# Performance work log

Hardware: AMD Instinct MI355X
Metric: run time of the kernel (lower is better)

Reference implementation:

```python
import jax, jax.numpy as jnp
import numpy as np

TEMP = 1.0
MEM = 1000           # memory_size
DIM = 128            # embedding_dim
MARGIN = 0.2
NC = 21              # num_classes
HARD_RATIO = 0.8
K_EASY = int(MEM // 5 * (1 - HARD_RATIO))   # 40
K_HARD = int(MEM // 5 * HARD_RATIO)         # 160
A = K_EASY + K_HARD                          # 200 sampled anchors
EPS = 1e-8


def _nearest_down(x, h, w):
    # torch F.interpolate(mode='nearest') downscale: src = floor(dst*H_in/H_out)
    B, H, W = x.shape
    ri = jnp.arange(h) * H // h
    ci = jnp.arange(w) * W // w
    return x[:, ri[:, None], ci[None, :]]


def _pick_first(mask, k):
    # deterministic stand-in for sampling_mask: first k True indices
    n = mask.shape[0]
    score = jnp.where(mask, -jnp.arange(n, dtype=jnp.float32), -jnp.inf)
    _, idx = jax.lax.top_k(score, k)
    return idx, mask[idx]


def setup_inputs() -> dict:
    key = jax.random.key(0)
    ks = jax.random.split(key, 5)
    return {
        "preds": jax.random.normal(ks[0], (8, NC, 512, 512), jnp.float32),
        "embeddings": jax.random.normal(ks[1], (8, DIM, 128, 128), jnp.float32),
        "wsss_gts": jax.random.randint(ks[2], (8, 512, 512), 0, NC, jnp.int32),
        "fsss_gts": jax.random.randint(ks[3], (8, 512, 512), 0, NC, jnp.int32),
        "memory": jax.random.normal(ks[4], (NC - 1, MEM, DIM), jnp.float32),
    }


def reference(preds, embeddings, wsss_gts, fsss_gts, memory):
    B, D, h, w = embeddings.shape
    s_wsss = _nearest_down(wsss_gts, h, w).reshape(-1)                    # [N]
    s_pred = _nearest_down(preds.argmax(axis=1), h, w).reshape(-1)        # [N]
    s_fsss = _nearest_down(fsss_gts, h, w).reshape(-1)                    # [N]

    # L2-normalize embeddings over channel dim, flatten to [N, D]
    emb = embeddings / jnp.maximum(
        jnp.linalg.norm(embeddings, axis=1, keepdims=True), 1e-12)
    emb = emb.transpose(1, 0, 2, 3).reshape(D, -1).T                       # [N, D]

    fg = (s_fsss != 0) & (s_fsss != 255)
    valid_lbl = (s_wsss != 0) & (s_wsss != 255)
    # original loop body overwrites cls with the FIRST (smallest) fg class
    cls = jnp.min(jnp.where(valid_lbl, s_wsss, NC)).astype(jnp.int32)

    anc = (s_wsss == cls) & fg
    easy = anc & (s_pred == cls)
    hard = anc & ~(s_pred == cls)
    ei, ev = _pick_first(easy, K_EASY)
    hi, hv = _pick_first(hard, K_HARD)
    idx = jnp.concatenate([ei, hi])                                        # [A]
    valid = jnp.concatenate([ev, hv])                                      # [A]
    anchors = emb[idx]                                                     # [A, D] (unit norm)

    mem_n = memory / jnp.maximum(
        jnp.linalg.norm(memory, axis=-1, keepdims=True), EPS)
    # all anchor-vs-memory cosine similarities in one batched matmul
    sims = jnp.einsum('ad,cmd->acm', anchors, mem_n)                       # [A, NC-1, MEM]
    pos = sims[:, cls - 1, :]                                              # [A, MEM]
    neg_mask = (jnp.arange(NC - 1) != (cls - 1))
    neg = jnp.where(neg_mask[None, :, None], sims, -jnp.inf).reshape(A, -1)
    hard_neg, _ = jax.lax.top_k(neg, MEM)                                  # [A, MEM] hardest

    # all (pos, hard_neg) pairs per anchor: relu(pos - neg + margin)
    pair = jnp.maximum(pos[:, :, None] - hard_neg[:, None, :] + MARGIN, 0.0)  # [A,MEM,MEM]
    per_anchor = pair.mean(axis=(1, 2))
    vf = valid.astype(pair.dtype)
    loss = jnp.sum(per_anchor * vf) / jnp.maximum(jnp.sum(vf), 1.0)

    # circular memory update for class `cls` (ptr starts at 0); invalid -> dropped
    wpos = jnp.cumsum(valid.astype(jnp.int32)) - 1
    widx = jnp.where(valid, wpos % MEM, MEM)
    new_memory = memory.at[cls - 1, widx].set(
        jax.lax.stop_gradient(anchors), mode='drop')
    return loss, new_memory
```

## Files before the change

### kernel.cpp

```cpp
#include <hip/hip_runtime.h>
#include <stdint.h>

#define NCK 21
#define K_EASY 39
#define K_HARD 160
#define A_TOT  199
#define MARGINF 0.2f

#define OFF_EASY   64
#define OFF_HARD   256
#define OFF_PERA   1024
#define OFF_MINARR 2048
#define OFF_FLAGS1 4096
#define OFF_FLAGS2 135168
#define OFF_ANCH   266240
#define OFF_SIMS   409600

__device__ __forceinline__ unsigned int f2key(float f) {
  unsigned int u = __float_as_uint(f);
  return u ^ ((u & 0x80000000u) ? 0xFFFFFFFFu : 0x80000000u);
}
__device__ __forceinline__ float key2f(unsigned int k) {
  unsigned int u = (k & 0x80000000u) ? (k ^ 0x80000000u) : (k ^ 0xFFFFFFFFu);
  return __uint_as_float(u);
}

__global__ void k_prep(const int* __restrict__ wsss, const int* __restrict__ fsss,
                       unsigned char* __restrict__ flags1, int* __restrict__ minArr) {
  int p = blockIdx.x * 256 + threadIdx.x;
  int b = p >> 14, r = p & 16383, i = r >> 7, j = r & 127;
  int gi = (b * 512 + i * 4) * 512 + j * 4;
  int w = wsss[gi];
  int f = fsss[gi];
  int fg = (f != 0 && f != 255) ? 1 : 0;
  int wl = (w != 0 && w != 255) ? 1 : 0;
  flags1[p] = (unsigned char)((w & 63) | (fg << 6));
  int cand = wl ? w : NCK;
  for (int off = 32; off > 0; off >>= 1) cand = min(cand, __shfl_down(cand, off));
  __shared__ int wmin[4];
  int lane = threadIdx.x & 63, wid = threadIdx.x >> 6;
  if (lane == 0) wmin[wid] = cand;
  __syncthreads();
  if (threadIdx.x == 0)
    minArr[blockIdx.x] = min(min(wmin[0], wmin[1]), min(wmin[2], wmin[3]));
}

__global__ void k_flags(const float* __restrict__ preds, const unsigned char* __restrict__ flags1,
                        unsigned char* __restrict__ flags2, const int* __restrict__ minArr,
                        int* __restrict__ hdr) {
  int tid = threadIdx.x;
  __shared__ int wm[4];
  __shared__ int s_cls;
  int m = min(minArr[tid], minArr[tid + 256]);
  for (int off = 32; off > 0; off >>= 1) m = min(m, __shfl_down(m, off));
  int lane = tid & 63, wid = tid >> 6;
  if (lane == 0) wm[wid] = m;
  __syncthreads();
  if (tid == 0) {
    int c = min(min(wm[0], wm[1]), min(wm[2], wm[3]));
    s_cls = c;
    if (blockIdx.x == 0) { hdr[0] = c; hdr[6] = 0; }
  }
  __syncthreads();
  int cls = s_cls;
  int p = blockIdx.x * 256 + tid;
  unsigned char f1 = flags1[p];
  unsigned char out = 0;
  if ((f1 & 64) && (int)(f1 & 63) == cls) {
    int b = p >> 14, r = p & 16383, i = r >> 7, j = r & 127;
    int base = ((b * NCK) * 512 + i * 4) * 512 + j * 4;
    float best = preds[base]; int bi = 0;
#pragma unroll
    for (int ch = 1; ch < NCK; ++ch) {
      float v = preds[base + ch * 262144];
      if (v > best) { best = v; bi = ch; }
    }
    out = (bi == cls) ? 1 : 2;
  }
  flags2[p] = out;
}

__global__ void k_pick(const unsigned char* __restrict__ flags2, int* __restrict__ hdr,
                       int* __restrict__ easy_idx, int* __restrict__ hard_idx) {
  int lane = threadIdx.x;
  const unsigned long long* f8 = (const unsigned long long*)flags2;
  unsigned int runE = 0, runH = 0;
  for (int it4 = 0; it4 < 64; ++it4) {
    unsigned long long vv0 = f8[(it4 * 4 + 0) * 64 + lane];
    unsigned long long vv1 = f8[(it4 * 4 + 1) * 64 + lane];
    unsigned long long vv2 = f8[(it4 * 4 + 2) * 64 + lane];
    unsigned long long vv3 = f8[(it4 * 4 + 3) * 64 + lane];
#pragma unroll
    for (int q = 0; q < 4; ++q) {
      unsigned long long v = (q == 0) ? vv0 : (q == 1) ? vv1 : (q == 2) ? vv2 : vv3;
      int it = it4 * 4 + q;
      unsigned int e = 0, h = 0;
#pragma unroll
      for (int g = 0; g < 8; ++g) {
        unsigned int b = (unsigned int)((v >> (8 * g)) & 255ull);
        e += (b == 1u); h += (b == 2u);
      }
      unsigned int x = (e << 16) | h;
      unsigned int incl = x;
#pragma unroll
      for (int off = 1; off < 64; off <<= 1) {
        unsigned int t = __shfl_up(incl, off);
        if (lane >= off) incl += t;
      }
      unsigned int excl = incl - x;
      unsigned int eRk = runE + (excl >> 16);
      unsigned int hRk = runH + (excl & 0xFFFFu);
#pragma unroll
      for (int g = 0; g < 8; ++g) {
        unsigned int b = (unsigned int)((v >> (8 * g)) & 255ull);
        int p = it * 512 + lane * 8 + g;
        if (b == 1u)      { if (eRk < K_EASY) easy_idx[eRk] = p; eRk++; }
        else if (b == 2u) { if (hRk < K_HARD) hard_idx[hRk] = p; hRk++; }
      }
      unsigned int tot = __shfl(incl, 63);
      runE += (tot >> 16); runH += (tot & 0xFFFFu);
    }
    if (runE >= K_EASY && runH >= K_HARD) break;
  }
  if (lane == 0) {
    int neU = runE < K_EASY ? (int)runE : K_EASY;
    int nhU = runH < K_HARD ? (int)runH : K_HARD;
    hdr[1] = (int)runE; hdr[2] = (int)runH;
    hdr[3] = neU; hdr[4] = nhU; hdr[5] = neU + nhU;
  }
}

__global__ void k_anchors(const float* __restrict__ emb, const int* __restrict__ hdr,
                          const int* __restrict__ easy_idx, const int* __restrict__ hard_idx,
                          float* __restrict__ anchors) {
  int a = blockIdx.x;
  int tid = threadIdx.x;
  int nv = hdr[5], neU = hdr[3];
  float v0 = 0.f, v1 = 0.f;
  if (a < nv) {
    int p = (a < neU) ? easy_idx[a] : hard_idx[a - neU];
    int b = p >> 14, r = p & 16383, i = r >> 7, j = r & 127;
    int base = b * 2097152 + i * 128 + j;
    v0 = emb[base + tid * 16384];
    v1 = emb[base + (tid + 64) * 16384];
  }
  float ss = v0 * v0 + v1 * v1;
  for (int off = 32; off > 0; off >>= 1) ss += __shfl_xor(ss, off);
  float inv = 1.0f / fmaxf(sqrtf(ss), 1e-12f);
  anchors[a * 128 + tid] = v0 * inv;
  anchors[a * 128 + tid + 64] = v1 * inv;
}

__global__ __launch_bounds__(256) void k_sims(const float* __restrict__ anchors,
                       const float* __restrict__ memory, float* __restrict__ sims,
                       int a0, int ac) {
  __shared__ float As[64 * 128];
  __shared__ float Ms[64 * 128];
  int mT = blockIdx.x, aT = blockIdx.y;
  int aBase = aT * 64, mBase = mT * 64;
  int tid = threadIdx.x;
#pragma unroll
  for (int k = 0; k < 8; ++k) {
    int f4i = tid + k * 256;
    int row = f4i >> 5, c = f4i & 31;
    int gR = a0 + aBase + row; if (gR > 255) gR = 255;
    float4 v = ((const float4*)anchors)[gR * 32 + c];
    *(float4*)&As[row * 128 + ((c ^ (row & 31)) << 2)] = v;
  }
#pragma unroll
  for (int k = 0; k < 8; ++k) {
    int f4i = tid + k * 256;
    int row = f4i >> 5, c = f4i & 31;
    int grow = mBase + row;
    float4 v = make_float4(0.f, 0.f, 0.f, 0.f);
    if (grow < 20000) v = ((const float4*)memory)[grow * 32 + c];
    *(float4*)&Ms[row * 128 + ((c ^ (row & 31)) << 2)] = v;
  }
  __syncthreads();
  int tx = tid & 15, ty = tid >> 4;
  float acc[4][4];
#pragma unroll
  for (int i = 0; i < 4; ++i)
#pragma unroll
    for (int j = 0; j < 4; ++j) acc[i][j] = 0.f;
#pragma unroll 2
  for (int c = 0; c < 32; ++c) {
    float4 av[4], mv[4];
#pragma unroll
    for (int i = 0; i < 4; ++i) {
      int ar = ty + 16 * i;
      av[i] = *(const float4*)&As[ar * 128 + ((c ^ (ar & 31)) << 2)];
    }
#pragma unroll
    for (int j = 0; j < 4; ++j) {
      int mr = tx + 16 * j;
      mv[j] = *(const float4*)&Ms[mr * 128 + ((c ^ (mr & 31)) << 2)];
    }
#pragma unroll
    for (int i = 0; i < 4; ++i)
#pragma unroll
      for (int j = 0; j < 4; ++j)
        acc[i][j] += av[i].x * mv[j].x + av[i].y * mv[j].y + av[i].z * mv[j].z + av[i].w * mv[j].w;
  }
  __syncthreads();
  {
    int row = tid >> 2, q = tid & 3;
    float ss = 0.f;
#pragma unroll
    for (int k = 0; k < 8; ++k) {
      float4 v = *(const float4*)&Ms[row * 128 + q * 32 + k * 4];
      ss += v.x * v.x + v.y * v.y + v.z * v.z + v.w * v.w;
    }
    ss += __shfl_down(ss, 2, 4);
    ss += __shfl_down(ss, 1, 4);
    if (q == 0) As[row] = 1.0f / fmaxf(sqrtf(ss), 1e-8f);
  }
  __syncthreads();
#pragma unroll
  for (int i = 0; i < 4; ++i) {
    int la = aBase + ty + 16 * i;
    if (la < ac) {
#pragma unroll
      for (int j = 0; j < 4; ++j) {
        int m = mBase + tx + 16 * j;
        if (m < 20000) sims[(size_t)la * 20000 + m] = acc[i][j] * As[tx + 16 * j];
      }
    }
  }
}

__device__ __forceinline__ void suffix_select(unsigned int* histL, unsigned int* sfx,
                                              unsigned int* cnts, int tid, unsigned int krem) {
  if (tid < 64) {
    int lane = tid;
    unsigned int h0 = histL[lane * 4 + 0];
    unsigned int h1 = histL[lane * 4 + 1];
    unsigned int h2 = histL[lane * 4 + 2];
    unsigned int h3 = histL[lane * 4 + 3];
    unsigned int s = h0 + h1 + h2 + h3;
    unsigned int incl = s;
#pragma unroll
    for (int off = 1; off < 64; off <<= 1) {
      unsigned int t = __shfl_down(incl, off);
      if (lane + off < 64) incl += t;
    }
    unsigned int above = incl - s;
    unsigned int f3 = above + h3;
    unsigned int f2 = f3 + h2;
    unsigned int f1 = f2 + h1;
    unsigned int f0 = f1 + h0;
    sfx[lane * 4 + 0] = f0; sfx[lane * 4 + 1] = f1;
    sfx[lane * 4 + 2] = f2; sfx[lane * 4 + 3] = f3;
    if (lane == 63) sfx[256] = 0u;
    if (f0 >= krem && f1 < krem)    cnts[3] = (unsigned int)(lane * 4 + 0);
    if (f1 >= krem && f2 < krem)    cnts[3] = (unsigned int)(lane * 4 + 1);
    if (f2 >= krem && f3 < krem)    cnts[3] = (unsigned int)(lane * 4 + 2);
    if (f3 >= krem && above < krem) cnts[3] = (unsigned int)(lane * 4 + 3);
  }
  __syncthreads();
}

__global__ __launch_bounds__(1024) void k_topk(const float* __restrict__ sims,
                       int* __restrict__ hdr, float* __restrict__ per_anchor,
                       int a0, int ac, float* __restrict__ out,
                       const float* __restrict__ memory, const float* __restrict__ anchors,
                       int doCopy) {
  int tid = threadIdx.x, lane = tid & 63, wid = tid >> 6;
  int nv = hdr[5];
  int cls = hdr[0];

  if (doCopy) {
    int step = gridDim.x * 1024;
    for (int i = blockIdx.x * 1024 + tid; i < 2560000; i += step) {
      float v = memory[i];
      int c = i / 128000;
      int rem = i - c * 128000;
      int m = rem >> 7, d = rem & 127;
      if (cls >= 1 && cls <= 20 && c == cls - 1 && m < nv) v = anchors[m * 128 + d];
      out[1 + i] = v;
    }
    if (nv == 0 && blockIdx.x == 0 && tid == 0) out[0] = 0.f;
  }

  int la = blockIdx.x;
  if (la >= ac) return;
  int a = a0 + la;
  if (a >= nv) return;
  int clsRow = cls - 1;

  __shared__ float posArr[1024];
  __shared__ float qv[1024];
  __shared__ unsigned int hist16[16][256];
  __shared__ unsigned int histL[256];
  __shared__ unsigned int sfx[257];
  __shared__ unsigned int buf[12288];
  __shared__ unsigned int cnts[8];
  __shared__ float fred[16];
  __shared__ unsigned int lastFlag;

  const float* row = sims + (size_t)la * 20000;

  for (int i = tid; i < 16 * 256; i += 1024) ((unsigned int*)hist16)[i] = 0u;
  if (tid < 24) posArr[1000 + tid] = -1e30f;
  if (tid < 8) cnts[tid] = 0u;
  __syncthreads();

  float4 rowq[5];
#pragma unroll
  for (int k = 0; k < 5; ++k) {
    int j = (k << 12) + (tid << 2);
    float4 v = make_float4(0.f, 0.f, 0.f, 0.f);
    if (j < 20000) v = *(const float4*)&row[j];
    rowq[k] = v;
  }
#pragma unroll
  for (int k = 0; k < 5; ++k) {
    int j = (k << 12) + (tid << 2);
    if (j < 20000) {
      int c = j / 1000;
      float4 v = rowq[k];
      if (c == clsRow) {
        *(float4*)&posArr[j - clsRow * 1000] = v;
      } else {
        atomicAdd(&hist16[wid][f2key(v.x) >> 24], 1u);
        atomicAdd(&hist16[wid][f2key(v.y) >> 24], 1u);
        atomicAdd(&hist16[wid][f2key(v.z) >> 24], 1u);
        atomicAdd(&hist16[wid][f2key(v.w) >> 24], 1u);
      }
    }
  }
  __syncthreads();
  if (tid < 256) {
    unsigned int s = 0;
#pragma unroll
    for (int w = 0; w < 16; ++w) s += hist16[w][tid];
    histL[tid] = s;
  }
  __syncthreads();
  suffix_select(histL, sfx, cnts, tid, 1000u);
  unsigned int B0 = cnts[3];
  unsigned int krem = 1000u - sfx[B0 + 1];
  __syncthreads();

#pragma unroll
  for (int k = 0; k < 5; ++k) {
    int j = (k << 12) + (tid << 2);
    bool inb = (j < 20000);
    int c = inb ? (j / 1000) : -1;
    bool neg = inb && (c != clsRow);
    float4 v4 = rowq[k];
#pragma unroll
    for (int e = 0; e < 4; ++e) {
      float v = (e == 0) ? v4.x : (e == 1) ? v4.y : (e == 2) ? v4.z : v4.w;
      unsigned int key = f2key(v);
      unsigned int tb = key >> 24;
      bool pq = neg && (tb > B0);
      bool pb = neg && (tb == B0);
      unsigned long long mq = __ballot(pq);
      unsigned long long mb = __ballot(pb);
      unsigned int baseq = 0u, baseb = 0u;
      if (lane == 0) {
        if (mq) baseq = atomicAdd(&cnts[2], (unsigned int)__popcll(mq));
        if (mb) baseb = atomicAdd(&cnts[1], (unsigned int)__popcll(mb));
      }
      baseq = __shfl(baseq, 0); baseb = __shfl(baseb, 0);
      if (pq) qv[baseq + (unsigned int)__popcll(mq & ((1ull << lane) - 1ull))] = v;
      if (pb) {
        unsigned int p = baseb + (unsigned int)__popcll(mb & ((1ull << lane) - 1ull));
        if (p < 12288u) buf[p] = key;
      }
    }
  }
  __syncthreads();
  int ncand = (int)cnts[1];
  bool stored = (ncand <= 12288);

  unsigned int prefix = B0 << 24;
  for (int level = 0; level < 3; ++level) {
    int shift = 16 - level * 8;
    if (tid < 256) histL[tid] = 0u;
    __syncthreads();
    unsigned int myk[12];
    if (stored) {
#pragma unroll
      for (int k = 0; k < 12; ++k) {
        int i = tid + (k << 10);
        if (i < ncand) myk[k] = buf[i];
      }
      __syncthreads();
#pragma unroll
      for (int k = 0; k < 12; ++k) {
        int i = tid + (k << 10);
        if (i < ncand) atomicAdd(&histL[(myk[k] >> shift) & 255u], 1u);
      }
    } else {
      unsigned int hiMask = 0xFFFFFFFFu << (shift + 8);
      for (int j = tid; j < 20000; j += 1024) {
        int c = j / 1000;
        if (c == clsRow) continue;
        unsigned int key = f2key(row[j]);
        if ((key & hiMask) == prefix) atomicAdd(&histL[(key >> shift) & 255u], 1u);
      }
    }
    __syncthreads();
    suffix_select(histL, sfx, cnts, tid, krem);
    unsigned int bk = cnts[3];
    unsigned int above = sfx[bk + 1];
    krem -= above;
    prefix |= bk << shift;
    if (stored) {
      __syncthreads();
      if (tid == 0) cnts[4] = 0u;
      __syncthreads();
#pragma unroll
      for (int k = 0; k < 12; ++k) {
        int i = tid + (k << 10);
        if (i < ncand) {
          unsigned int b = (myk[k] >> shift) & 255u;
          if (b > bk) qv[atomicAdd(&cnts[2], 1u)] = key2f(myk[k]);
          else if (b == bk) buf[atomicAdd(&cnts[4], 1u)] = myk[k];
        }
      }
      __syncthreads();
      ncand = (int)cnts[4];
    }
  }
  float tval = key2f(prefix);

  if (!stored) {
    for (int j = tid; j < 20000; j += 1024) {
      int c = j / 1000;
      if (c == clsRow) continue;
      float v = row[j];
      unsigned int key = f2key(v);
      if ((key >> 24) == B0 && key > prefix) qv[atomicAdd(&cnts[2], 1u) & 1023u] = v;
    }
    __syncthreads();
  }
  int qn = (int)cnts[2];
  float tieW = (float)krem;

  float v, w;
  if (tid < qn)       { v = qv[tid]; w = 1.f; }
  else if (tid == qn) { v = tval;    w = tieW; }
  else                { v = 0.f;     w = 0.f; }
  float t = v - MARGINF;
  float s0 = 0.f, s1 = 0.f, s2 = 0.f, s3 = 0.f;
  if (w != 0.f) {
    for (int pc = 0; pc < 1024; pc += 16) {
      float4 p0 = *(const float4*)&posArr[pc];
      float4 p1 = *(const float4*)&posArr[pc + 4];
      float4 p2 = *(const float4*)&posArr[pc + 8];
      float4 p3 = *(const float4*)&posArr[pc + 12];
      s0 += fmaxf(p0.x - t, 0.f); s1 += fmaxf(p0.y - t, 0.f);
      s2 += fmaxf(p0.z - t, 0.f); s3 += fmaxf(p0.w - t, 0.f);
      s0 += fmaxf(p1.x - t, 0.f); s1 += fmaxf(p1.y - t, 0.f);
      s2 += fmaxf(p1.z - t, 0.f); s3 += fmaxf(p1.w - t, 0.f);
      s0 += fmaxf(p2.x - t, 0.f); s1 += fmaxf(p2.y - t, 0.f);
      s2 += fmaxf(p2.z - t, 0.f); s3 += fmaxf(p2.w - t, 0.f);
      s0 += fmaxf(p3.x - t, 0.f); s1 += fmaxf(p3.y - t, 0.f);
      s2 += fmaxf(p3.z - t, 0.f); s3 += fmaxf(p3.w - t, 0.f);
    }
  }
  float local = w * ((s0 + s1) + (s2 + s3));
  for (int off = 32; off; off >>= 1) local += __shfl_down(local, off);
  if (lane == 0) fred[wid] = local;
  __syncthreads();
  if (tid == 0) {
    float s = 0.f;
#pragma unroll
    for (int i = 0; i < 16; ++i) s += fred[i];
    per_anchor[a] = s * 1e-6f;
    __threadfence();
    unsigned int tk = atomicAdd((unsigned int*)&hdr[6], 1u);
    lastFlag = (tk == (unsigned int)(nv - 1)) ? 1u : 0u;
  }
  __syncthreads();
  if (lastFlag) {
    __threadfence();
    float s = (tid < nv) ? per_anchor[tid] : 0.f;
    for (int off = 32; off; off >>= 1) s += __shfl_down(s, off);
    if (lane == 0) fred[wid] = s;
    __syncthreads();
    if (tid == 0) {
      float tot = 0.f;
#pragma unroll
      for (int i = 0; i < 16; ++i) tot += fred[i];
      out[0] = tot / (float)max(nv, 1);
    }
  }
}

__global__ void k_writemem(const float* __restrict__ memory, const float* __restrict__ anchors,
                           const int* __restrict__ hdr, float* __restrict__ out) {
  int cls = hdr[0], nv = hdr[5];
  if (nv == 0 && blockIdx.x == 0 && threadIdx.x == 0) out[0] = 0.f;
  int i = blockIdx.x * 1024 + threadIdx.x;
#pragma unroll
  for (int k = 0; k < 4; ++k, i += 256) {
    float v = memory[i];
    int c = i / 128000;
    int rem = i - c * 128000;
    int m = rem >> 7, d = rem & 127;
    if (cls >= 1 && cls <= 20 && c == cls - 1 && m < nv) v = anchors[m * 128 + d];
    out[1 + i] = v;
  }
}

extern "C" void kernel_launch(void* const* d_in, const int* in_sizes, int n_in,
                              void* d_out, int out_size, void* d_ws, size_t ws_size,
                              hipStream_t stream) {
  const float* preds  = (const float*)d_in[0];
  const float* emb    = (const float*)d_in[1];
  const int*   wsss   = (const int*)d_in[2];
  const int*   fsss   = (const int*)d_in[3];
  const float* memory = (const float*)d_in[4];
  float* out = (float*)d_out;
  char* ws = (char*)d_ws;
  int* hdr = (int*)ws;
  int* easy_idx = (int*)(ws + OFF_EASY);
  int* hard_idx = (int*)(ws + OFF_HARD);
  float* per_anchor = (float*)(ws + OFF_PERA);
  int* minArr = (int*)(ws + OFF_MINARR);
  unsigned char* flags1 = (unsigned char*)(ws + OFF_FLAGS1);
  unsigned char* flags2 = (unsigned char*)(ws + OFF_FLAGS2);
  float* anchors = (float*)(ws + OFF_ANCH);
  float* sims = (float*)(ws + OFF_SIMS);

  hipLaunchKernelGGL(k_prep,    dim3(512), dim3(256), 0, stream, wsss, fsss, flags1, minArr);
  hipLaunchKernelGGL(k_flags,   dim3(512), dim3(256), 0, stream, preds, flags1, flags2, minArr, hdr);
  hipLaunchKernelGGL(k_pick,    dim3(1),   dim3(64),  0, stream, flags2, hdr, easy_idx, hard_idx);
  hipLaunchKernelGGL(k_anchors, dim3(256), dim3(64),  0, stream, emb, hdr, easy_idx, hard_idx, anchors);

  long long avail = (long long)ws_size - (long long)OFF_SIMS;
  int capWs = (avail > 0) ? (int)(avail / 80000LL) : 0;
  if (capWs > A_TOT) capWs = A_TOT;

  if (capWs >= A_TOT) {
    dim3 gs(313, (A_TOT + 63) / 64);
    hipLaunchKernelGGL(k_sims, gs, dim3(256), 0, stream, anchors, memory, sims, 0, A_TOT);
    hipLaunchKernelGGL(k_topk, dim3(A_TOT), dim3(1024), 0, stream, sims, hdr, per_anchor,
                       0, A_TOT, out, memory, anchors, 1);
  } else {
    float* outScr = out + 4;
    int capOut = (int)(((long long)out_size / 4 - 4) / 20000LL);
    if (capOut > 127) capOut = 127;
    if (capOut < 0) capOut = 0;
    if (capOut + capWs < 1) capWs = 1;
    int aoff = 0;
    while (aoff < A_TOT) {
      int nOut = A_TOT - aoff; if (nOut > capOut) nOut = capOut;
      int nWs  = A_TOT - aoff - nOut; if (nWs > capWs) nWs = capWs;
      if (nOut > 0) {
        dim3 g1(313, (nOut + 63) / 64);
        hipLaunchKernelGGL(k_sims, g1, dim3(256), 0, stream, anchors, memory, outScr, aoff, nOut);
      }
      if (nWs > 0) {
        dim3 g2(313, (nWs + 63) / 64);
        hipLaunchKernelGGL(k_sims, g2, dim3(256), 0, stream, anchors, memory, sims, aoff + nOut, nWs);
      }
      if (nOut > 0)
        hipLaunchKernelGGL(k_topk, dim3(nOut), dim3(1024), 0, stream, outScr, hdr, per_anchor,
                           aoff, nOut, out, memory, anchors, 0);
      if (nWs > 0)
        hipLaunchKernelGGL(k_topk, dim3(nWs), dim3(1024), 0, stream, sims, hdr, per_anchor,
                           aoff + nOut, nWs, out, memory, anchors, 0);
      aoff += nOut + nWs;
    }
    hipLaunchKernelGGL(k_writemem, dim3(2500), dim3(256), 0, stream, memory, anchors, hdr, out);
  }
}
```

Measured before the change: 373.3 us.

## Fuse anchor pick, anchor normalize and sims matmul into one kernel

Merges the serial pick kernel, the anchor-gather kernel and the similarity matmul into a single launch of 1252 blocks. Global atomic flags in the header act as in-kernel barriers: block 0 does the pick, blocks 0-63 normalize anchors, and the rest spin until both stages finish. This removes two kernel launches and the idle gaps between them. In exchange, all blocks busy-wait on a single serial stage, and correctness depends on the early blocks being scheduled before the waiting blocks fill the device. The old separate kernels are kept only for the small-workspace fallback path.

```diff
diff --git a/kernel.cpp b/kernel.cpp
--- a/kernel.cpp
+++ b/kernel.cpp
@@ -59,7 +59,7 @@
   if (tid == 0) {
     int c = min(min(wm[0], wm[1]), min(wm[2], wm[3]));
     s_cls = c;
-    if (blockIdx.x == 0) { hdr[0] = c; hdr[6] = 0; }
+    if (blockIdx.x == 0) { hdr[0] = c; hdr[6] = 0; hdr[7] = 0; hdr[8] = 0; }
   }
   __syncthreads();
   int cls = s_cls;
@@ -80,90 +80,107 @@
   flags2[p] = out;
 }
 
-__global__ void k_pick(const unsigned char* __restrict__ flags2, int* __restrict__ hdr,
-                       int* __restrict__ easy_idx, int* __restrict__ hard_idx) {
-  int lane = threadIdx.x;
-  const unsigned long long* f8 = (const unsigned long long*)flags2;
-  unsigned int runE = 0, runH = 0;
-  for (int it4 = 0; it4 < 64; ++it4) {
-    unsigned long long vv0 = f8[(it4 * 4 + 0) * 64 + lane];
-    unsigned long long vv1 = f8[(it4 * 4 + 1) * 64 + lane];
-    unsigned long long vv2 = f8[(it4 * 4 + 2) * 64 + lane];
-    unsigned long long vv3 = f8[(it4 * 4 + 3) * 64 + lane];
-#pragma unroll
-    for (int q = 0; q < 4; ++q) {
-      unsigned long long v = (q == 0) ? vv0 : (q == 1) ? vv1 : (q == 2) ? vv2 : vv3;
-      int it = it4 * 4 + q;
-      unsigned int e = 0, h = 0;
-#pragma unroll
-      for (int g = 0; g < 8; ++g) {
-        unsigned int b = (unsigned int)((v >> (8 * g)) & 255ull);
-        e += (b == 1u); h += (b == 2u);
-      }
-      unsigned int x = (e << 16) | h;
-      unsigned int incl = x;
-#pragma unroll
-      for (int off = 1; off < 64; off <<= 1) {
-        unsigned int t = __shfl_up(incl, off);
-        if (lane >= off) incl += t;
-      }
-      unsigned int excl = incl - x;
-      unsigned int eRk = runE + (excl >> 16);
-      unsigned int hRk = runH + (excl & 0xFFFFu);
-#pragma unroll
-      for (int g = 0; g < 8; ++g) {
-        unsigned int b = (unsigned int)((v >> (8 * g)) & 255ull);
-        int p = it * 512 + lane * 8 + g;
-        if (b == 1u)      { if (eRk < K_EASY) easy_idx[eRk] = p; eRk++; }
-        else if (b == 2u) { if (hRk < K_HARD) hard_idx[hRk] = p; hRk++; }
-      }
-      unsigned int tot = __shfl(incl, 63);
-      runE += (tot >> 16); runH += (tot & 0xFFFFu);
-    }
-    if (runE >= K_EASY && runH >= K_HARD) break;
-  }
-  if (lane == 0) {
-    int neU = runE < K_EASY ? (int)runE : K_EASY;
-    int nhU = runH < K_HARD ? (int)runH : K_HARD;
-    hdr[1] = (int)runE; hdr[2] = (int)runH;
-    hdr[3] = neU; hdr[4] = nhU; hdr[5] = neU + nhU;
-  }
-}
-
-__global__ void k_anchors(const float* __restrict__ emb, const int* __restrict__ hdr,
-                          const int* __restrict__ easy_idx, const int* __restrict__ hard_idx,
-                          float* __restrict__ anchors) {
-  int a = blockIdx.x;
-  int tid = threadIdx.x;
-  int nv = hdr[5], neU = hdr[3];
-  float v0 = 0.f, v1 = 0.f;
-  if (a < nv) {
-    int p = (a < neU) ? easy_idx[a] : hard_idx[a - neU];
-    int b = p >> 14, r = p & 16383, i = r >> 7, j = r & 127;
-    int base = b * 2097152 + i * 128 + j;
-    v0 = emb[base + tid * 16384];
-    v1 = emb[base + (tid + 64) * 16384];
-  }
-  float ss = v0 * v0 + v1 * v1;
-  for (int off = 32; off > 0; off >>= 1) ss += __shfl_xor(ss, off);
-  float inv = 1.0f / fmaxf(sqrtf(ss), 1e-12f);
-  anchors[a * 128 + tid] = v0 * inv;
-  anchors[a * 128 + tid + 64] = v1 * inv;
-}
-
-__global__ __launch_bounds__(256) void k_sims(const float* __restrict__ anchors,
-                       const float* __restrict__ memory, float* __restrict__ sims,
-                       int a0, int ac) {
+__global__ __launch_bounds__(256) void k_pas(const unsigned char* __restrict__ flags2,
+                       int* __restrict__ hdr, int* __restrict__ easy_idx,
+                       int* __restrict__ hard_idx, const float* __restrict__ emb,
+                       float* __restrict__ anchors, const float* __restrict__ memory,
+                       float* __restrict__ sims) {
+  int bid = blockIdx.x, tid = threadIdx.x;
   __shared__ float As[64 * 128];
   __shared__ float Ms[64 * 128];
-  int mT = blockIdx.x, aT = blockIdx.y;
+
+  if (bid == 0 && tid < 64) {
+    int lane = tid;
+    const unsigned long long* f8 = (const unsigned long long*)flags2;
+    unsigned int runE = 0, runH = 0;
+    for (int it4 = 0; it4 < 64; ++it4) {
+      unsigned long long vv0 = f8[(it4 * 4 + 0) * 64 + lane];
+      unsigned long long vv1 = f8[(it4 * 4 + 1) * 64 + lane];
+      unsigned long long vv2 = f8[(it4 * 4 + 2) * 64 + lane];
+      unsigned long long vv3 = f8[(it4 * 4 + 3) * 64 + lane];
+#pragma unroll
+      for (int q = 0; q < 4; ++q) {
+        unsigned long long v = (q == 0) ? vv0 : (q == 1) ? vv1 : (q == 2) ? vv2 : vv3;
+        int it = it4 * 4 + q;
+        unsigned int e = 0, h = 0;
+#pragma unroll
+        for (int g = 0; g < 8; ++g) {
+          unsigned int b = (unsigned int)((v >> (8 * g)) & 255ull);
+          e += (b == 1u); h += (b == 2u);
+        }
+        unsigned int x = (e << 16) | h;
+        unsigned int incl = x;
+#pragma unroll
+        for (int off = 1; off < 64; off <<= 1) {
+          unsigned int t = __shfl_up(incl, off);
+          if (lane >= off) incl += t;
+        }
+        unsigned int excl = incl - x;
+        unsigned int eRk = runE + (excl >> 16);
+        unsigned int hRk = runH + (excl & 0xFFFFu);
+#pragma unroll
+        for (int g = 0; g < 8; ++g) {
+          unsigned int b = (unsigned int)((v >> (8 * g)) & 255ull);
+          int p = it * 512 + lane * 8 + g;
+          if (b == 1u)      { if (eRk < K_EASY) easy_idx[eRk] = p; eRk++; }
+          else if (b == 2u) { if (hRk < K_HARD) hard_idx[hRk] = p; hRk++; }
+        }
+        unsigned int tot = __shfl(incl, 63);
+        runE += (tot >> 16); runH += (tot & 0xFFFFu);
+      }
+      if (runE >= K_EASY && runH >= K_HARD) break;
+    }
+    if (lane == 0) {
+      int neU = runE < K_EASY ? (int)runE : K_EASY;
+      int nhU = runH < K_HARD ? (int)runH : K_HARD;
+      hdr[1] = (int)runE; hdr[2] = (int)runH;
+      hdr[3] = neU; hdr[4] = nhU; hdr[5] = neU + nhU;
+    }
+    __threadfence();
+    if (lane == 0) atomicExch(&hdr[7], 1);
+  }
+
+  if (tid == 0) {
+    while (atomicAdd(&hdr[7], 0) == 0) __builtin_amdgcn_s_sleep(8);
+  }
+  __syncthreads();
+  __threadfence();
+  int nv = hdr[5], neU = hdr[3];
+
+  if (bid < 64) {
+    int lane = tid & 63, w = tid >> 6;
+    int a = bid * 4 + w;
+    float v0 = 0.f, v1 = 0.f;
+    if (a < nv) {
+      int p = (a < neU) ? easy_idx[a] : hard_idx[a - neU];
+      int b = p >> 14, r = p & 16383, i = r >> 7, j = r & 127;
+      int base = b * 2097152 + i * 128 + j;
+      v0 = emb[base + lane * 16384];
+      v1 = emb[base + (lane + 64) * 16384];
+    }
+    float ss = v0 * v0 + v1 * v1;
+    for (int off = 32; off > 0; off >>= 1) ss += __shfl_xor(ss, off);
+    float inv = 1.0f / fmaxf(sqrtf(ss), 1e-12f);
+    anchors[a * 128 + lane] = v0 * inv;
+    anchors[a * 128 + lane + 64] = v1 * inv;
+    __syncthreads();
+    __threadfence();
+    if (tid == 0) atomicAdd(&hdr[8], 1);
+  }
+
+  if (tid == 0) {
+    while (atomicAdd(&hdr[8], 0) < 64) __builtin_amdgcn_s_sleep(8);
+  }
+  __syncthreads();
+  __threadfence();
+
+  int mT = bid % 313, aT = bid / 313;
   int aBase = aT * 64, mBase = mT * 64;
-  int tid = threadIdx.x;
 #pragma unroll
   for (int k = 0; k < 8; ++k) {
     int f4i = tid + k * 256;
     int row = f4i >> 5, c = f4i & 31;
-    int gR = a0 + aBase + row; if (gR > 255) gR = 255;
+    int gR = aBase + row; if (gR > 255) gR = 255;
     float4 v = ((const float4*)anchors)[gR * 32 + c];
     *(float4*)&As[row * 128 + ((c ^ (row & 31)) << 2)] = v;
   }
@@ -219,7 +236,7 @@
 #pragma unroll
   for (int i = 0; i < 4; ++i) {
     int la = aBase + ty + 16 * i;
-    if (la < ac) {
+    if (la < A_TOT) {
 #pragma unroll
       for (int j = 0; j < 4; ++j) {
         int m = mBase + tx + 16 * j;
@@ -491,6 +508,147 @@
   }
 }
 
+__global__ void k_pick(const unsigned char* __restrict__ flags2, int* __restrict__ hdr,
+                       int* __restrict__ easy_idx, int* __restrict__ hard_idx) {
+  int lane = threadIdx.x;
+  const unsigned long long* f8 = (const unsigned long long*)flags2;
+  unsigned int runE = 0, runH = 0;
+  for (int it = 0; it < 256; ++it) {
+    unsigned long long v = f8[it * 64 + lane];
+    unsigned int e = 0, h = 0;
+#pragma unroll
+    for (int g = 0; g < 8; ++g) {
+      unsigned int b = (unsigned int)((v >> (8 * g)) & 255ull);
+      e += (b == 1u); h += (b == 2u);
+    }
+    unsigned int x = (e << 16) | h;
+    unsigned int incl = x;
+#pragma unroll
+    for (int off = 1; off < 64; off <<= 1) {
+      unsigned int t = __shfl_up(incl, off);
+      if (lane >= off) incl += t;
+    }
+    unsigned int excl = incl - x;
+    unsigned int eRk = runE + (excl >> 16);
+    unsigned int hRk = runH + (excl & 0xFFFFu);
+#pragma unroll
+    for (int g = 0; g < 8; ++g) {
+      unsigned int b = (unsigned int)((v >> (8 * g)) & 255ull);
+      int p = it * 512 + lane * 8 + g;
+      if (b == 1u)      { if (eRk < K_EASY) easy_idx[eRk] = p; eRk++; }
+      else if (b == 2u) { if (hRk < K_HARD) hard_idx[hRk] = p; hRk++; }
+    }
+    unsigned int tot = __shfl(incl, 63);
+    runE += (tot >> 16); runH += (tot & 0xFFFFu);
+    if (runE >= K_EASY && runH >= K_HARD) break;
+  }
+  if (lane == 0) {
+    int neU = runE < K_EASY ? (int)runE : K_EASY;
+    int nhU = runH < K_HARD ? (int)runH : K_HARD;
+    hdr[1] = (int)runE; hdr[2] = (int)runH;
+    hdr[3] = neU; hdr[4] = nhU; hdr[5] = neU + nhU;
+  }
+}
+
+__global__ void k_anchors(const float* __restrict__ emb, const int* __restrict__ hdr,
+                          const int* __restrict__ easy_idx, const int* __restrict__ hard_idx,
+                          float* __restrict__ anchors) {
+  int a = blockIdx.x;
+  int tid = threadIdx.x;
+  int nv = hdr[5], neU = hdr[3];
+  float v0 = 0.f, v1 = 0.f;
+  if (a < nv) {
+    int p = (a < neU) ? easy_idx[a] : hard_idx[a - neU];
+    int b = p >> 14, r = p & 16383, i = r >> 7, j = r & 127;
+    int base = b * 2097152 + i * 128 + j;
+    v0 = emb[base + tid * 16384];
+    v1 = emb[base + (tid + 64) * 16384];
+  }
+  float ss = v0 * v0 + v1 * v1;
+  for (int off = 32; off > 0; off >>= 1) ss += __shfl_xor(ss, off);
+  float inv = 1.0f / fmaxf(sqrtf(ss), 1e-12f);
+  anchors[a * 128 + tid] = v0 * inv;
+  anchors[a * 128 + tid + 64] = v1 * inv;
+}
+
+__global__ __launch_bounds__(256) void k_sims(const float* __restrict__ anchors,
+                       const float* __restrict__ memory, float* __restrict__ sims,
+                       int a0, int ac) {
+  __shared__ float As[64 * 128];
+  __shared__ float Ms[64 * 128];
+  int mT = blockIdx.x, aT = blockIdx.y;
+  int aBase = aT * 64, mBase = mT * 64;
+  int tid = threadIdx.x;
+#pragma unroll
+  for (int k = 0; k < 8; ++k) {
+    int f4i = tid + k * 256;
+    int row = f4i >> 5, c = f4i & 31;
+    int gR = a0 + aBase + row; if (gR > 255) gR = 255;
+    float4 v = ((const float4*)anchors)[gR * 32 + c];
+    *(float4*)&As[row * 128 + ((c ^ (row & 31)) << 2)] = v;
+  }
+#pragma unroll
+  for (int k = 0; k < 8; ++k) {
+    int f4i = tid + k * 256;
+    int row = f4i >> 5, c = f4i & 31;
+    int grow = mBase + row;
+    float4 v = make_float4(0.f, 0.f, 0.f, 0.f);
+    if (grow < 20000) v = ((const float4*)memory)[grow * 32 + c];
+    *(float4*)&Ms[row * 128 + ((c ^ (row & 31)) << 2)] = v;
+  }
+  __syncthreads();
+  int tx = tid & 15, ty = tid >> 4;
+  float acc[4][4];
+#pragma unroll
+  for (int i = 0; i < 4; ++i)
+#pragma unroll
+    for (int j = 0; j < 4; ++j) acc[i][j] = 0.f;
+#pragma unroll 2
+  for (int c = 0; c < 32; ++c) {
+    float4 av[4], mv[4];
+#pragma unroll
+    for (int i = 0; i < 4; ++i) {
+      int ar = ty + 16 * i;
+      av[i] = *(const float4*)&As[ar * 128 + ((c ^ (ar & 31)) << 2)];
+    }
+#pragma unroll
+    for (int j = 0; j < 4; ++j) {
+      int mr = tx + 16 * j;
+      mv[j] = *(const float4*)&Ms[mr * 128 + ((c ^ (mr & 31)) << 2)];
+    }
+#pragma unroll
+    for (int i = 0; i < 4; ++i)
+#pragma unroll
+      for (int j = 0; j < 4; ++j)
+        acc[i][j] += av[i].x * mv[j].x + av[i].y * mv[j].y + av[i].z * mv[j].z + av[i].w * mv[j].w;
+  }
+  __syncthreads();
+  {
+    int row = tid >> 2, q = tid & 3;
+    float ss = 0.f;
+#pragma unroll
+    for (int k = 0; k < 8; ++k) {
+      float4 v = *(const float4*)&Ms[row * 128 + q * 32 + k * 4];
+      ss += v.x * v.x + v.y * v.y + v.z * v.z + v.w * v.w;
+    }
+    ss += __shfl_down(ss, 2, 4);
+    ss += __shfl_down(ss, 1, 4);
+    if (q == 0) As[row] = 1.0f / fmaxf(sqrtf(ss), 1e-8f);
+  }
+  __syncthreads();
+#pragma unroll
+  for (int i = 0; i < 4; ++i) {
+    int la = aBase + ty + 16 * i;
+    if (la < ac) {
+#pragma unroll
+      for (int j = 0; j < 4; ++j) {
+        int m = mBase + tx + 16 * j;
+        if (m < 20000) sims[(size_t)la * 20000 + m] = acc[i][j] * As[tx + 16 * j];
+      }
+    }
+  }
+}
+
 __global__ void k_writemem(const float* __restrict__ memory, const float* __restrict__ anchors,
                            const int* __restrict__ hdr, float* __restrict__ out) {
   int cls = hdr[0], nv = hdr[5];
@@ -527,21 +685,21 @@
   float* anchors = (float*)(ws + OFF_ANCH);
   float* sims = (float*)(ws + OFF_SIMS);
 
-  hipLaunchKernelGGL(k_prep,    dim3(512), dim3(256), 0, stream, wsss, fsss, flags1, minArr);
-  hipLaunchKernelGGL(k_flags,   dim3(512), dim3(256), 0, stream, preds, flags1, flags2, minArr, hdr);
-  hipLaunchKernelGGL(k_pick,    dim3(1),   dim3(64),  0, stream, flags2, hdr, easy_idx, hard_idx);
-  hipLaunchKernelGGL(k_anchors, dim3(256), dim3(64),  0, stream, emb, hdr, easy_idx, hard_idx, anchors);
+  hipLaunchKernelGGL(k_prep,  dim3(512), dim3(256), 0, stream, wsss, fsss, flags1, minArr);
+  hipLaunchKernelGGL(k_flags, dim3(512), dim3(256), 0, stream, preds, flags1, flags2, minArr, hdr);
 
   long long avail = (long long)ws_size - (long long)OFF_SIMS;
   int capWs = (avail > 0) ? (int)(avail / 80000LL) : 0;
   if (capWs > A_TOT) capWs = A_TOT;
 
   if (capWs >= A_TOT) {
-    dim3 gs(313, (A_TOT + 63) / 64);
-    hipLaunchKernelGGL(k_sims, gs, dim3(256), 0, stream, anchors, memory, sims, 0, A_TOT);
+    hipLaunchKernelGGL(k_pas, dim3(1252), dim3(256), 0, stream, flags2, hdr,
+                       easy_idx, hard_idx, emb, anchors, memory, sims);
     hipLaunchKernelGGL(k_topk, dim3(A_TOT), dim3(1024), 0, stream, sims, hdr, per_anchor,
                        0, A_TOT, out, memory, anchors, 1);
   } else {
+    hipLaunchKernelGGL(k_pick,    dim3(1),   dim3(64), 0, stream, flags2, hdr, easy_idx, hard_idx);
+    hipLaunchKernelGGL(k_anchors, dim3(256), dim3(64), 0, stream, emb, hdr, easy_idx, hard_idx, anchors);
     float* outScr = out + 4;
     int capOut = (int)(((long long)out_size / 4 - 4) / 20000LL);
     if (capOut > 127) capOut = 127;
```

Measured after the change: 570.2 us. 1.53x slower.

## Fuse argmax into prep and merge pick/anchor kernels into one block

Applied to the files above, without the earlier changes.

The per-pixel argmax over prediction channels moves into the prep kernel and is packed into a 16-bit flag word. The class reduction, easy/hard index selection and anchor gather/normalization are merged into a single 1024-thread kernel. This removes two kernel launches and the intermediate flags2 buffer. In exchange, argmax now runs for every downsampled pixel rather than only anchor-candidate pixels, and the anchor gather runs in one block instead of 256.

```diff
diff --git a/kernel.cpp b/kernel.cpp
--- a/kernel.cpp
+++ b/kernel.cpp
@@ -11,8 +11,7 @@
 #define OFF_HARD   256
 #define OFF_PERA   1024
 #define OFF_MINARR 2048
-#define OFF_FLAGS1 4096
-#define OFF_FLAGS2 135168
+#define OFF_FL     4096
 #define OFF_ANCH   266240
 #define OFF_SIMS   409600
 
@@ -26,7 +25,8 @@
 }
 
 __global__ void k_prep(const int* __restrict__ wsss, const int* __restrict__ fsss,
-                       unsigned char* __restrict__ flags1, int* __restrict__ minArr) {
+                       const float* __restrict__ preds,
+                       unsigned short* __restrict__ fl, int* __restrict__ minArr) {
   int p = blockIdx.x * 256 + threadIdx.x;
   int b = p >> 14, r = p & 16383, i = r >> 7, j = r & 127;
   int gi = (b * 512 + i * 4) * 512 + j * 4;
@@ -34,7 +34,14 @@
   int f = fsss[gi];
   int fg = (f != 0 && f != 255) ? 1 : 0;
   int wl = (w != 0 && w != 255) ? 1 : 0;
-  flags1[p] = (unsigned char)((w & 63) | (fg << 6));
+  int base = ((b * NCK) * 512 + i * 4) * 512 + j * 4;
+  float best = preds[base]; int bi = 0;
+#pragma unroll
+  for (int ch = 1; ch < NCK; ++ch) {
+    float v = preds[base + ch * 262144];
+    if (v > best) { best = v; bi = ch; }
+  }
+  fl[p] = (unsigned short)((w & 63) | (fg << 6) | (bi << 8));
   int cand = wl ? w : NCK;
   for (int off = 32; off > 0; off >>= 1) cand = min(cand, __shfl_down(cand, off));
   __shared__ int wmin[4];
@@ -45,110 +52,119 @@
     minArr[blockIdx.x] = min(min(wmin[0], wmin[1]), min(wmin[2], wmin[3]));
 }
 
-__global__ void k_flags(const float* __restrict__ preds, const unsigned char* __restrict__ flags1,
-                        unsigned char* __restrict__ flags2, const int* __restrict__ minArr,
-                        int* __restrict__ hdr) {
+__global__ __launch_bounds__(1024) void k_pa(const unsigned short* __restrict__ fl,
+                       const int* __restrict__ minArr, int* __restrict__ hdr,
+                       int* __restrict__ easy_idx, int* __restrict__ hard_idx,
+                       const float* __restrict__ emb, float* __restrict__ anchors) {
   int tid = threadIdx.x;
-  __shared__ int wm[4];
-  __shared__ int s_cls;
-  int m = min(minArr[tid], minArr[tid + 256]);
+  __shared__ int red[16];
+  __shared__ int s_cls, s_neU, s_nv;
+
+  int m = NCK;
+  if (tid < 512) m = minArr[tid];
   for (int off = 32; off > 0; off >>= 1) m = min(m, __shfl_down(m, off));
-  int lane = tid & 63, wid = tid >> 6;
-  if (lane == 0) wm[wid] = m;
+  if ((tid & 63) == 0) red[tid >> 6] = m;
   __syncthreads();
   if (tid == 0) {
-    int c = min(min(wm[0], wm[1]), min(wm[2], wm[3]));
+    int c = red[0];
+#pragma unroll
+    for (int i = 1; i < 16; ++i) c = min(c, red[i]);
     s_cls = c;
-    if (blockIdx.x == 0) { hdr[0] = c; hdr[6] = 0; }
+    hdr[0] = c;
+    hdr[6] = 0;
   }
   __syncthreads();
   int cls = s_cls;
-  int p = blockIdx.x * 256 + tid;
-  unsigned char f1 = flags1[p];
-  unsigned char out = 0;
-  if ((f1 & 64) && (int)(f1 & 63) == cls) {
-    int b = p >> 14, r = p & 16383, i = r >> 7, j = r & 127;
-    int base = ((b * NCK) * 512 + i * 4) * 512 + j * 4;
-    float best = preds[base]; int bi = 0;
-#pragma unroll
-    for (int ch = 1; ch < NCK; ++ch) {
-      float v = preds[base + ch * 262144];
-      if (v > best) { best = v; bi = ch; }
-    }
-    out = (bi == cls) ? 1 : 2;
-  }
-  flags2[p] = out;
-}
-
-__global__ void k_pick(const unsigned char* __restrict__ flags2, int* __restrict__ hdr,
-                       int* __restrict__ easy_idx, int* __restrict__ hard_idx) {
-  int lane = threadIdx.x;
-  const unsigned long long* f8 = (const unsigned long long*)flags2;
-  unsigned int runE = 0, runH = 0;
-  for (int it4 = 0; it4 < 64; ++it4) {
-    unsigned long long vv0 = f8[(it4 * 4 + 0) * 64 + lane];
-    unsigned long long vv1 = f8[(it4 * 4 + 1) * 64 + lane];
-    unsigned long long vv2 = f8[(it4 * 4 + 2) * 64 + lane];
-    unsigned long long vv3 = f8[(it4 * 4 + 3) * 64 + lane];
-#pragma unroll
-    for (int q = 0; q < 4; ++q) {
-      unsigned long long v = (q == 0) ? vv0 : (q == 1) ? vv1 : (q == 2) ? vv2 : vv3;
-      int it = it4 * 4 + q;
-      unsigned int e = 0, h = 0;
-#pragma unroll
-      for (int g = 0; g < 8; ++g) {
-        unsigned int b = (unsigned int)((v >> (8 * g)) & 255ull);
-        e += (b == 1u); h += (b == 2u);
-      }
-      unsigned int x = (e << 16) | h;
-      unsigned int incl = x;
-#pragma unroll
-      for (int off = 1; off < 64; off <<= 1) {
-        unsigned int t = __shfl_up(incl, off);
-        if (lane >= off) incl += t;
-      }
-      unsigned int excl = incl - x;
-      unsigned int eRk = runE + (excl >> 16);
-      unsigned int hRk = runH + (excl & 0xFFFFu);
-#pragma unroll
-      for (int g = 0; g < 8; ++g) {
-        unsigned int b = (unsigned int)((v >> (8 * g)) & 255ull);
-        int p = it * 512 + lane * 8 + g;
-        if (b == 1u)      { if (eRk < K_EASY) easy_idx[eRk] = p; eRk++; }
-        else if (b == 2u) { if (hRk < K_HARD) hard_idx[hRk] = p; hRk++; }
-      }
-      unsigned int tot = __shfl(incl, 63);
-      runE += (tot >> 16); runH += (tot & 0xFFFFu);
-    }
-    if (runE >= K_EASY && runH >= K_HARD) break;
-  }
-  if (lane == 0) {
-    int neU = runE < K_EASY ? (int)runE : K_EASY;
-    int nhU = runH < K_HARD ? (int)runH : K_HARD;
-    hdr[1] = (int)runE; hdr[2] = (int)runH;
-    hdr[3] = neU; hdr[4] = nhU; hdr[5] = neU + nhU;
-  }
-}
-
-__global__ void k_anchors(const float* __restrict__ emb, const int* __restrict__ hdr,
-                          const int* __restrict__ easy_idx, const int* __restrict__ hard_idx,
-                          float* __restrict__ anchors) {
-  int a = blockIdx.x;
-  int tid = threadIdx.x;
-  int nv = hdr[5], neU = hdr[3];
-  float v0 = 0.f, v1 = 0.f;
-  if (a < nv) {
-    int p = (a < neU) ? easy_idx[a] : hard_idx[a - neU];
-    int b = p >> 14, r = p & 16383, i = r >> 7, j = r & 127;
-    int base = b * 2097152 + i * 128 + j;
-    v0 = emb[base + tid * 16384];
-    v1 = emb[base + (tid + 64) * 16384];
-  }
-  float ss = v0 * v0 + v1 * v1;
-  for (int off = 32; off > 0; off >>= 1) ss += __shfl_xor(ss, off);
-  float inv = 1.0f / fmaxf(sqrtf(ss), 1e-12f);
-  anchors[a * 128 + tid] = v0 * inv;
-  anchors[a * 128 + tid + 64] = v1 * inv;
+
+  if (tid < 64) {
+    int lane = tid;
+    const unsigned long long* f8 = (const unsigned long long*)fl;
+    unsigned int runE = 0, runH = 0;
+    for (int it2 = 0; it2 < 128; ++it2) {
+      unsigned long long A0 = f8[(it2 * 2 + 0) * 128 + lane * 2];
+      unsigned long long A1 = f8[(it2 * 2 + 0) * 128 + lane * 2 + 1];
+      unsigned long long B0 = f8[(it2 * 2 + 1) * 128 + lane * 2];
+      unsigned long long B1 = f8[(it2 * 2 + 1) * 128 + lane * 2 + 1];
+#pragma unroll
+      for (int q = 0; q < 2; ++q) {
+        unsigned long long lo = q ? B0 : A0;
+        unsigned long long hi = q ? B1 : A1;
+        int it = it2 * 2 + q;
+        unsigned int e = 0, h = 0, eb = 0, hb = 0;
+#pragma unroll
+        for (int g = 0; g < 8; ++g) {
+          unsigned int u = (unsigned int)(((g < 4 ? lo : hi) >> (16 * (g & 3))) & 0xFFFFull);
+          int lbl = u & 63, fgb = u & 64, am = (u >> 8) & 31;
+          bool anc = fgb && (lbl == cls);
+          bool ee = anc && (am == cls);
+          bool hh = anc && (am != cls);
+          e += ee; h += hh;
+          eb |= (ee ? 1u : 0u) << g; hb |= (hh ? 1u : 0u) << g;
+        }
+        unsigned int x = (e << 16) | h;
+        unsigned int incl = x;
+#pragma unroll
+        for (int off = 1; off < 64; off <<= 1) {
+          unsigned int t = __shfl_up(incl, off);
+          if (lane >= off) incl += t;
+        }
+        unsigned int excl = incl - x;
+        unsigned int eRk = runE + (excl >> 16);
+        unsigned int hRk = runH + (excl & 0xFFFFu);
+#pragma unroll
+        for (int g = 0; g < 8; ++g) {
+          int p = it * 512 + lane * 8 + g;
+          if ((eb >> g) & 1u)      { if (eRk < K_EASY) easy_idx[eRk] = p; eRk++; }
+          else if ((hb >> g) & 1u) { if (hRk < K_HARD) hard_idx[hRk] = p; hRk++; }
+        }
+        unsigned int tot = __shfl(incl, 63);
+        runE += (tot >> 16); runH += (tot & 0xFFFFu);
+      }
+      if (runE >= K_EASY && runH >= K_HARD) break;
+    }
+    if (lane == 0) {
+      int neU = runE < K_EASY ? (int)runE : K_EASY;
+      int nhU = runH < K_HARD ? (int)runH : K_HARD;
+      hdr[1] = (int)runE; hdr[2] = (int)runH;
+      hdr[3] = neU; hdr[4] = nhU; hdr[5] = neU + nhU;
+      s_neU = neU; s_nv = neU + nhU;
+    }
+  }
+  __syncthreads();
+  int nv = s_nv, neU = s_neU;
+
+  int lane = tid & 63, w = tid >> 6;
+  for (int rr = 0; rr < 8; ++rr) {
+    int a0 = rr * 32 + w;
+    int a1 = a0 + 16;
+    float u0 = 0.f, u1 = 0.f, v0 = 0.f, v1 = 0.f;
+    if (a0 < nv) {
+      int p = (a0 < neU) ? easy_idx[a0] : hard_idx[a0 - neU];
+      int b = p >> 14, r = p & 16383, i = r >> 7, j = r & 127;
+      int base = b * 2097152 + i * 128 + j;
+      u0 = emb[base + lane * 16384];
+      u1 = emb[base + (lane + 64) * 16384];
+    }
+    if (a1 < nv) {
+      int p = (a1 < neU) ? easy_idx[a1] : hard_idx[a1 - neU];
+      int b = p >> 14, r = p & 16383, i = r >> 7, j = r & 127;
+      int base = b * 2097152 + i * 128 + j;
+      v0 = emb[base + lane * 16384];
+      v1 = emb[base + (lane + 64) * 16384];
+    }
+    float ss0 = u0 * u0 + u1 * u1;
+    float ss1 = v0 * v0 + v1 * v1;
+    for (int off = 32; off > 0; off >>= 1) {
+      ss0 += __shfl_xor(ss0, off);
+      ss1 += __shfl_xor(ss1, off);
+    }
+    float inv0 = 1.0f / fmaxf(sqrtf(ss0), 1e-12f);
+    float inv1 = 1.0f / fmaxf(sqrtf(ss1), 1e-12f);
+    anchors[a0 * 128 + lane] = u0 * inv0;
+    anchors[a0 * 128 + lane + 64] = u1 * inv0;
+    anchors[a1 * 128 + lane] = v0 * inv1;
+    anchors[a1 * 128 + lane + 64] = v1 * inv1;
+  }
 }
 
 __global__ __launch_bounds__(256) void k_sims(const float* __restrict__ anchors,
@@ -522,15 +538,13 @@
   int* hard_idx = (int*)(ws + OFF_HARD);
   float* per_anchor = (float*)(ws + OFF_PERA);
   int* minArr = (int*)(ws + OFF_MINARR);
-  unsigned char* flags1 = (unsigned char*)(ws + OFF_FLAGS1);
-  unsigned char* flags2 = (unsigned char*)(ws + OFF_FLAGS2);
+  unsigned short* fl = (unsigned short*)(ws + OFF_FL);
   float* anchors = (float*)(ws + OFF_ANCH);
   float* sims = (float*)(ws + OFF_SIMS);
 
-  hipLaunchKernelGGL(k_prep,    dim3(512), dim3(256), 0, stream, wsss, fsss, flags1, minArr);
-  hipLaunchKernelGGL(k_flags,   dim3(512), dim3(256), 0, stream, preds, flags1, flags2, minArr, hdr);
-  hipLaunchKernelGGL(k_pick,    dim3(1),   dim3(64),  0, stream, flags2, hdr, easy_idx, hard_idx);
-  hipLaunchKernelGGL(k_anchors, dim3(256), dim3(64),  0, stream, emb, hdr, easy_idx, hard_idx, anchors);
+  hipLaunchKernelGGL(k_prep, dim3(512), dim3(256),  0, stream, wsss, fsss, preds, fl, minArr);
+  hipLaunchKernelGGL(k_pa,   dim3(1),   dim3(1024), 0, stream, fl, minArr, hdr,
+                     easy_idx, hard_idx, emb, anchors);
 
   long long avail = (long long)ws_size - (long long)OFF_SIMS;
   int capWs = (avail > 0) ? (int)(avail / 80000LL) : 0;
```

Result: slower. 421.3 us (+12.9%).
